# Performance work log

Hardware: AMD Instinct MI355X
Metric: run time of the kernel (lower is better)

## Reference

```python
import jax, jax.numpy as jnp
import numpy as np

D_MODEL = 768; D_KV = 64; H = 12; D_FF = 3072; L = 2
TP = 4; SP = 16; MT = 16; MS = 4
MASK_RATE = 0.2; EPS = 1e-6
B = 256; T = 64; F = 64
ST = (T // TP) * (F // SP)  # 64 tokens


def ln(x, s, b):
    mu = jnp.mean(x, -1, keepdims=True)
    var = jnp.mean(jnp.square(x - mu), -1, keepdims=True)
    return (x - mu) * jax.lax.rsqrt(var + EPS) * s + b


def mha(x, Wq, bq, Wk, bk, Wv, bv, Wo, bo):
    Bz, S, D = x.shape
    q = (x @ Wq + bq).reshape(Bz, S, H, D_KV)
    k = (x @ Wk + bk).reshape(Bz, S, H, D_KV)
    v = (x @ Wv + bv).reshape(Bz, S, H, D_KV)
    scores = jnp.einsum('bqhd,bkhd->bhqk', q, k) * (D_KV ** -0.5)
    attn = jax.nn.softmax(scores, axis=-1)
    o = jnp.einsum('bhqk,bkhd->bqhd', attn, v).reshape(Bz, S, H * D_KV)
    return o @ Wo + bo


def setup_inputs():
    key = jax.random.key(0)
    ks = jax.random.split(key, 16)
    s = 0.02
    nrm = lambda k, shp: jax.random.normal(k, shp, jnp.float32) * s
    return {
        'inputs': jax.random.normal(ks[0], (B, T, F, 1), jnp.float32),
        'randomness': jax.random.uniform(ks[1], (B * ST, 3), jnp.float32),
        'perm': jax.random.permutation(ks[2], B * ST),
        'conv_w': nrm(ks[3], (TP, SP, 1, D_MODEL)), 'conv_b': jnp.zeros((D_MODEL,)),
        'temp_embd': nrm(ks[4], (MT, D_MODEL)), 'spec_embd': nrm(ks[5], (MS, D_MODEL)),
        'pos_ln_s': jnp.ones((D_MODEL,)), 'pos_ln_b': jnp.zeros((D_MODEL,)),
        'mask_tok': nrm(ks[6], (D_MODEL,)), 'agg_tok': nrm(ks[7], (D_MODEL,)),
        'Wq': nrm(ks[8], (L, D_MODEL, H * D_KV)), 'bq': jnp.zeros((L, H * D_KV)),
        'Wk': nrm(ks[9], (L, D_MODEL, H * D_KV)), 'bk': jnp.zeros((L, H * D_KV)),
        'Wv': nrm(ks[10], (L, D_MODEL, H * D_KV)), 'bv': jnp.zeros((L, H * D_KV)),
        'Wo': nrm(ks[11], (L, H * D_KV, D_MODEL)), 'bo': jnp.zeros((L, D_MODEL)),
        'ln1_s': jnp.ones((L, D_MODEL)), 'ln1_b': jnp.zeros((L, D_MODEL)),
        'W1': nrm(ks[12], (L, D_MODEL, D_FF)), 'b1': jnp.zeros((L, D_FF)),
        'W2': nrm(ks[13], (L, D_FF, D_MODEL)), 'b2': jnp.zeros((L, D_MODEL)),
        'ln2_s': jnp.ones((L, D_MODEL)), 'ln2_b': jnp.zeros((L, D_MODEL)),
    }


def reference(inputs, randomness, perm, conv_w, conv_b, temp_embd, spec_embd,
              pos_ln_s, pos_ln_b, mask_tok, agg_tok, Wq, bq, Wk, bk, Wv, bv,
              Wo, bo, ln1_s, ln1_b, W1, b1, W2, b2, ln2_s, ln2_b):
    # Conv2D patchify: [B, T, F, 1] -> [B, T/4, F/16, d_model]
    x = jax.lax.conv_general_dilated(
        inputs, conv_w, (TP, SP), 'VALID',
        dimension_numbers=('NHWC', 'HWIO', 'NHWC')) + conv_b
    Bz, Tt, Ss, D = x.shape
    e = x.reshape(Bz, Tt * Ss, D)  # token embeddings [B, 64, 768]
    # Vectorized BERT-style random masking (replaces the per-element sparse-scatter loop)
    sel = randomness[:, 0] <= MASK_RATE
    m = (sel & (randomness[:, 1] <= 0.8)).astype(e.dtype).reshape(Bz, Tt * Ss)
    rnd = (sel & (randomness[:, 1] > 0.8) & (randomness[:, 2] <= 0.5)).astype(e.dtype).reshape(Bz, Tt * Ss)
    shuffled = jax.lax.stop_gradient(e.reshape(-1, D))[perm].reshape(Bz, Tt * Ss, D)
    me = e * (1.0 - m - rnd)[..., None] + mask_tok * m[..., None] + shuffled * rnd[..., None]
    # Spectro-temporal position embeddings + LN
    pos = (temp_embd[:Tt, None, :] + spec_embd[None, :Ss, :]).reshape(Tt * Ss, D)
    h = ln(me + pos, pos_ln_s, pos_ln_b)
    # Prepend AGG token
    h = jnp.concatenate([jnp.broadcast_to(agg_tok, (Bz, 1, D)), h], axis=1)
    # Post-norm transformer encoder
    for l in range(L):
        a = mha(h, Wq[l], bq[l], Wk[l], bk[l], Wv[l], bv[l], Wo[l], bo[l])
        h = ln(h + a, ln1_s[l], ln1_b[l])
        f = jax.nn.gelu(h @ W1[l] + b1[l], approximate=False) @ W2[l] + b2[l]
        h = ln(h + f, ln2_s[l], ln2_b[l])
    return h  # last_hidden_states [B, 65, 768]; aggregated=h[:,0], predictions=h[:,1:]
```

## Files before the change

kernel.cpp:

```cpp
#include <hip/hip_runtime.h>
#include <hip/hip_bf16.h>
#include <math.h>

using bf16 = __hip_bfloat16;
typedef __bf16 bf16x8v __attribute__((ext_vector_type(8)));
typedef float f32x4 __attribute__((ext_vector_type(4)));
typedef unsigned short ushort4v __attribute__((ext_vector_type(4)));

__device__ __forceinline__ float b2f(bf16 x) { return __bfloat162float(x); }
__device__ __forceinline__ bf16 f2b(float x) { return __float2bfloat16(x); }

__device__ __forceinline__ void gload_lds16(const void* g, void* l) {
  __builtin_amdgcn_global_load_lds(
      (__attribute__((address_space(1))) void*)(void*)g,
      (__attribute__((address_space(3))) void*)l, 16, 0, 0);
}

__device__ __forceinline__ float block_sum(float v, float* buf) {
  #pragma unroll
  for (int off = 32; off > 0; off >>= 1) v += __shfl_xor(v, off);
  __syncthreads();
  if ((threadIdx.x & 63) == 0) buf[threadIdx.x >> 6] = v;
  __syncthreads();
  return buf[0] + buf[1] + buf[2] + buf[3];
}

__global__ __launch_bounds__(256) void transpose_kernel(
    const float* __restrict__ in, bf16* __restrict__ out, int K, int N) {
  __shared__ float tile[32][33];
  const int nbx = N >> 5;
  const int bx = blockIdx.x % nbx, by = blockIdx.x / nbx;
  const int tx = threadIdx.x & 31, ty = threadIdx.x >> 5;
  #pragma unroll
  for (int i = 0; i < 4; ++i) {
    const int r = by * 32 + ty + i * 8;
    tile[ty + i * 8][tx] = in[(size_t)r * N + bx * 32 + tx];
  }
  __syncthreads();
  #pragma unroll
  for (int i = 0; i < 4; ++i) {
    const int r = bx * 32 + ty + i * 8;
    out[(size_t)r * K + by * 32 + tx] = f2b(tile[tx][ty + i * 8]);
  }
}

__global__ __launch_bounds__(256) void biasqkv_kernel(
    const float* __restrict__ bq, const float* __restrict__ bk,
    const float* __restrict__ bv, float* __restrict__ out) {
  const int i = blockIdx.x * 256 + threadIdx.x;
  if (i >= 2 * 2304) return;
  const int l = i / 2304, n = i % 2304;
  float v = (n < 768) ? bq[l * 768 + n]
          : (n < 1536) ? bk[l * 768 + n - 768] : bv[l * 768 + n - 1536];
  out[i] = v;
}

__global__ __launch_bounds__(256) void patchify_kernel(
    const float* __restrict__ in, const float* __restrict__ w,
    const float* __restrict__ cb, bf16* __restrict__ e) {
  __shared__ float patch[8][64];
  const int tid = threadIdx.x;
  const int tok0 = blockIdx.x * 8;
  for (int idx = tid; idx < 512; idx += 256) {
    const int t = idx >> 6, p = idx & 63;
    const int tok = tok0 + t;
    const int b = tok >> 6, t2 = tok & 63, tt = t2 >> 2, ss = t2 & 3;
    const int kt = p >> 4, kf = p & 15;
    patch[t][p] = in[((size_t)b * 64 + tt * 4 + kt) * 64 + ss * 16 + kf];
  }
  __syncthreads();
  for (int i = 0; i < 3; ++i) {
    const int d = tid + i * 256;
    const float cbv = cb[d];
    float acc[8];
    #pragma unroll
    for (int t = 0; t < 8; ++t) acc[t] = cbv;
    for (int p = 0; p < 64; ++p) {
      const float wv = w[p * 768 + d];
      #pragma unroll
      for (int t = 0; t < 8; ++t) acc[t] += patch[t][p] * wv;
    }
    #pragma unroll
    for (int t = 0; t < 8; ++t) e[(size_t)(tok0 + t) * 768 + d] = f2b(acc[t]);
  }
}

__global__ __launch_bounds__(256) void embed_kernel(
    const bf16* __restrict__ e, const float* __restrict__ randomness,
    const int* __restrict__ perm, const float* __restrict__ temp_embd,
    const float* __restrict__ spec_embd, const float* __restrict__ pls,
    const float* __restrict__ plb, const float* __restrict__ mask_tok,
    const float* __restrict__ agg_tok, bf16* __restrict__ h) {
  __shared__ float rbuf[4];
  const int row = blockIdx.x;
  const int b = row / 65, s = row % 65;
  const int tid = threadIdx.x;
  const size_t ob = (size_t)row * 768;
  if (s == 0) {
    #pragma unroll
    for (int i = 0; i < 3; ++i) { const int d = tid + i * 256; h[ob + d] = f2b(agg_tok[d]); }
    return;
  }
  const int tok = s - 1;
  const int gt = b * 64 + tok;
  const float r0 = randomness[gt * 3 + 0];
  const float r1 = randomness[gt * 3 + 1];
  const float r2 = randomness[gt * 3 + 2];
  const bool selb = (r0 <= 0.2f);
  const bool mflag = selb && (r1 <= 0.8f);
  const bool rflag = selb && (r1 > 0.8f) && (r2 <= 0.5f);
  const int src = rflag ? perm[gt] : gt;
  const int tt = tok >> 2, ss2 = tok & 3;
  float v[3]; float sum = 0.f;
  #pragma unroll
  for (int i = 0; i < 3; ++i) {
    const int d = tid + i * 256;
    const float ev = mflag ? mask_tok[d] : b2f(e[(size_t)src * 768 + d]);
    v[i] = ev + temp_embd[tt * 768 + d] + spec_embd[ss2 * 768 + d];
    sum += v[i];
  }
  const float mu = block_sum(sum, rbuf) * (1.f / 768.f);
  float q = 0.f;
  #pragma unroll
  for (int i = 0; i < 3; ++i) { const float t = v[i] - mu; q += t * t; }
  const float rstd = rsqrtf(block_sum(q, rbuf) * (1.f / 768.f) + 1e-6f);
  #pragma unroll
  for (int i = 0; i < 3; ++i) {
    const int d = tid + i * 256;
    h[ob + d] = f2b((v[i] - mu) * rstd * pls[d] + plb[d]);
  }
}

template <int F32OUT>
__global__ __launch_bounds__(256) void resln_kernel(
    const bf16* __restrict__ x, const bf16* __restrict__ y,
    const float* __restrict__ sc, const float* __restrict__ bi,
    void* __restrict__ outp) {
  __shared__ float rbuf[4];
  const int tid = threadIdx.x;
  const size_t base = (size_t)blockIdx.x * 768;
  float v[3]; float s = 0.f;
  #pragma unroll
  for (int i = 0; i < 3; ++i) {
    const int d = tid + i * 256;
    v[i] = b2f(x[base + d]) + b2f(y[base + d]);
    s += v[i];
  }
  const float mu = block_sum(s, rbuf) * (1.f / 768.f);
  float q = 0.f;
  #pragma unroll
  for (int i = 0; i < 3; ++i) { const float t = v[i] - mu; q += t * t; }
  const float rstd = rsqrtf(block_sum(q, rbuf) * (1.f / 768.f) + 1e-6f);
  #pragma unroll
  for (int i = 0; i < 3; ++i) {
    const int d = tid + i * 256;
    const float o = (v[i] - mu) * rstd * sc[d] + bi[d];
    if (F32OUT) ((float*)outp)[base + d] = o;
    else        ((bf16*)outp)[base + d] = f2b(o);
  }
}

template <int ACT>
__global__ __launch_bounds__(256, 2) void gemm_bt_kernel(
    const unsigned short* __restrict__ A, const unsigned short* __restrict__ BT,
    const float* __restrict__ bias, bf16* __restrict__ C, int N, int K) {
  __shared__ __align__(16) unsigned short lA[128 * 32];
  __shared__ __align__(16) unsigned short lB[128 * 32];
  const int tid = threadIdx.x;
  const int wid = tid >> 6, lane = tid & 63;
  const int nbn = N >> 7;
  const int bm = blockIdx.x / nbn, bn = blockIdx.x % nbn;
  const int wm = (wid >> 1) << 6, wn = (wid & 1) << 6;

  const size_t Kb = (size_t)K * 2;
  const char* gA = (const char*)A + (size_t)bm * 128 * Kb;
  const char* gB = (const char*)BT + (size_t)bn * 128 * Kb;
  const int r0 = tid >> 2;
  const int c0 = (tid & 3) * 16;
  char* lAw = (char*)lA + wid * 1024;
  char* lBw = (char*)lB + wid * 1024;

  const f32x4 z = {0.f, 0.f, 0.f, 0.f};
  f32x4 acc[4][4];
  #pragma unroll
  for (int i = 0; i < 4; ++i)
    #pragma unroll
    for (int j = 0; j < 4; ++j) acc[i][j] = z;

  const int frow = lane & 15;
  const int koff = (lane >> 4) * 8;

  for (int k0 = 0; k0 < K; k0 += 32) {
    const char* ga = gA + (size_t)k0 * 2 + c0;
    const char* gb = gB + (size_t)k0 * 2 + c0;
    gload_lds16(ga + (size_t)r0 * Kb, lAw);
    gload_lds16(ga + (size_t)(r0 + 64) * Kb, lAw + 4096);
    gload_lds16(gb + (size_t)r0 * Kb, lBw);
    gload_lds16(gb + (size_t)(r0 + 64) * Kb, lBw + 4096);
    __syncthreads();
    bf16x8v af[4], bfv[4];
    #pragma unroll
    for (int m = 0; m < 4; ++m)
      af[m] = *(const bf16x8v*)&lA[(wm + m * 16 + frow) * 32 + koff];
    #pragma unroll
    for (int n = 0; n < 4; ++n)
      bfv[n] = *(const bf16x8v*)&lB[(wn + n * 16 + frow) * 32 + koff];
    #pragma unroll
    for (int m = 0; m < 4; ++m)
      #pragma unroll
      for (int n = 0; n < 4; ++n)
        acc[m][n] = __builtin_amdgcn_mfma_f32_16x16x32_bf16(af[m], bfv[n], acc[m][n], 0, 0, 0);
    __syncthreads();
  }

  const int row0 = bm * 128 + wm + ((lane >> 4) << 2);
  const int col0 = bn * 128 + wn + frow;
  #pragma unroll
  for (int n = 0; n < 4; ++n) {
    const int col = col0 + n * 16;
    const float bv = bias[col];
    #pragma unroll
    for (int m = 0; m < 4; ++m) {
      const int row = row0 + m * 16;
      #pragma unroll
      for (int r = 0; r < 4; ++r) {
        float v = acc[m][n][r] + bv;
        if (ACT == 1) v = 0.5f * v * (1.0f + erff(v * 0.70710678f));
        C[(size_t)(row + r) * N + col] = f2b(v);
      }
    }
  }
}

__global__ __launch_bounds__(320) void attn_mfma_kernel(
    const bf16* __restrict__ qkv, bf16* __restrict__ ctx) {
  __shared__ __align__(16) bf16 sK[80][72];
  __shared__ __align__(16) bf16 sVt[64][104];
  __shared__ __align__(16) bf16 sP[5][16][104];
  const int b = blockIdx.x / 12, h = blockIdx.x % 12;
  const int tid = threadIdx.x;
  const int wave = tid >> 6, lane = tid & 63;
  const size_t base = ((size_t)b * 65) * 2304 + (size_t)h * 64;
  const bf16 bzero = f2b(0.f);

  for (int idx = tid; idx < 65 * 16; idx += 320) {
    const int row = idx >> 4, d4 = (idx & 15) * 4;
    const ushort4v kv = *(const ushort4v*)(qkv + base + (size_t)row * 2304 + 768 + d4);
    const ushort4v vv = *(const ushort4v*)(qkv + base + (size_t)row * 2304 + 1536 + d4);
    *(ushort4v*)&sK[row][d4] = kv;
    #pragma unroll
    for (int j = 0; j < 4; ++j) ((unsigned short*)&sVt[d4 + j][row])[0] = vv[j];
  }
  for (int idx = tid; idx < 15 * 16; idx += 320) {
    const int row = 65 + (idx >> 4), d4 = (idx & 15) * 4;
    *(ushort4v*)&sK[row][d4] = ushort4v{0, 0, 0, 0};
  }
  for (int idx = tid; idx < 64 * 8; idx += 320) {
    const int d = idx >> 3, c4 = 64 + (idx & 7) * 4;
    (void)d; (void)c4;
  }
  for (int idx = tid; idx < 64 * 31; idx += 320) {
    const int d = idx / 31, c = 65 + (idx % 31);
    sVt[d][c] = bzero;
  }
  __syncthreads();

  const int frow = lane & 15;
  const int koff = (lane >> 4) * 8;
  const int row0 = wave * 16;
  const int qrow = (row0 + frow > 64) ? 64 : (row0 + frow);
  const bf16* qptr = qkv + base + (size_t)qrow * 2304;
  const bf16x8v aq0 = *(const bf16x8v*)(qptr + koff);
  const bf16x8v aq1 = *(const bf16x8v*)(qptr + 32 + koff);

  const f32x4 z4 = {0.f, 0.f, 0.f, 0.f};
  f32x4 sacc[5];
  #pragma unroll
  for (int n = 0; n < 5; ++n) sacc[n] = z4;
  #pragma unroll
  for (int n = 0; n < 5; ++n) {
    const bf16x8v b0 = *(const bf16x8v*)&sK[n * 16 + frow][koff];
    const bf16x8v b1 = *(const bf16x8v*)&sK[n * 16 + frow][32 + koff];
    sacc[n] = __builtin_amdgcn_mfma_f32_16x16x32_bf16(aq0, b0, sacc[n], 0, 0, 0);
    sacc[n] = __builtin_amdgcn_mfma_f32_16x16x32_bf16(aq1, b1, sacc[n], 0, 0, 0);
  }

  #pragma unroll
  for (int r = 0; r < 4; ++r) {
    const int prow = ((lane >> 4) << 2) + r;
    float v[5];
    float mx = -1e30f;
    #pragma unroll
    for (int n = 0; n < 5; ++n) {
      const int col = n * 16 + frow;
      v[n] = (col < 65) ? sacc[n][r] * 0.125f : -1e30f;
      mx = fmaxf(mx, v[n]);
    }
    #pragma unroll
    for (int off = 1; off < 16; off <<= 1) mx = fmaxf(mx, __shfl_xor(mx, off));
    float sum = 0.f;
    #pragma unroll
    for (int n = 0; n < 5; ++n) { v[n] = __expf(v[n] - mx); sum += v[n]; }
    #pragma unroll
    for (int off = 1; off < 16; off <<= 1) sum += __shfl_xor(sum, off);
    const float inv = 1.f / sum;
    #pragma unroll
    for (int n = 0; n < 5; ++n)
      sP[wave][prow][n * 16 + frow] = f2b(v[n] * inv);
    sP[wave][prow][80 + frow] = bzero;
  }

  f32x4 oacc[4];
  #pragma unroll
  for (int n = 0; n < 4; ++n) oacc[n] = z4;
  #pragma unroll
  for (int kk = 0; kk < 3; ++kk) {
    const bf16x8v ap = *(const bf16x8v*)&sP[wave][frow][kk * 32 + koff];
    #pragma unroll
    for (int n = 0; n < 4; ++n) {
      const bf16x8v bv = *(const bf16x8v*)&sVt[n * 16 + frow][kk * 32 + koff];
      oacc[n] = __builtin_amdgcn_mfma_f32_16x16x32_bf16(ap, bv, oacc[n], 0, 0, 0);
    }
  }

  #pragma unroll
  for (int r = 0; r < 4; ++r) {
    const int row = row0 + ((lane >> 4) << 2) + r;
    if (row < 65) {
      bf16* op = ctx + ((size_t)b * 65 + row) * 768 + (size_t)h * 64 + frow;
      #pragma unroll
      for (int n = 0; n < 4; ++n) op[n * 16] = f2b(oacc[n][r]);
    }
  }
}

extern "C" void kernel_launch(void* const* d_in, const int* in_sizes, int n_in,
                              void* d_out, int out_size, void* d_ws, size_t ws_size,
                              hipStream_t stream) {
  (void)in_sizes; (void)n_in; (void)out_size; (void)ws_size;
  const float* inputs     = (const float*)d_in[0];
  const float* randomness = (const float*)d_in[1];
  const int*   perm       = (const int*)d_in[2];
  const float* conv_w     = (const float*)d_in[3];
  const float* conv_b     = (const float*)d_in[4];
  const float* temp_embd  = (const float*)d_in[5];
  const float* spec_embd  = (const float*)d_in[6];
  const float* pos_ln_s   = (const float*)d_in[7];
  const float* pos_ln_b   = (const float*)d_in[8];
  const float* mask_tok   = (const float*)d_in[9];
  const float* agg_tok    = (const float*)d_in[10];
  const float* Wq = (const float*)d_in[11]; const float* bq = (const float*)d_in[12];
  const float* Wk = (const float*)d_in[13]; const float* bk = (const float*)d_in[14];
  const float* Wv = (const float*)d_in[15]; const float* bv = (const float*)d_in[16];
  const float* Wo = (const float*)d_in[17]; const float* bo = (const float*)d_in[18];
  const float* ln1_s = (const float*)d_in[19]; const float* ln1_b = (const float*)d_in[20];
  const float* W1 = (const float*)d_in[21]; const float* b1 = (const float*)d_in[22];
  const float* W2 = (const float*)d_in[23]; const float* b2 = (const float*)d_in[24];
  const float* ln2_s = (const float*)d_in[25]; const float* ln2_b = (const float*)d_in[26];

  char* wsb = (char*)d_ws;
  size_t off = 0;
  auto carve = [&](size_t bytes) { char* p = wsb + off; off = (off + bytes + 255) & ~(size_t)255; return p; };
  bf16* wqkvT = (bf16*)carve((size_t)2 * 2304 * 768 * 2);
  bf16* woT   = (bf16*)carve((size_t)2 * 768 * 768 * 2);
  bf16* w1T   = (bf16*)carve((size_t)2 * 3072 * 768 * 2);
  bf16* w2T   = (bf16*)carve((size_t)2 * 768 * 3072 * 2);
  float* bqkv = (float*)carve((size_t)2 * 2304 * 4);
  bf16* ebuf  = (bf16*)carve((size_t)16640 * 768 * 2);
  bf16* hbuf  = (bf16*)carve((size_t)16640 * 768 * 2);
  bf16* qkvb  = (bf16*)carve((size_t)16640 * 2304 * 2);
  bf16* ctxb  = (bf16*)carve((size_t)16640 * 768 * 2);
  bf16* tmpb  = ebuf;
  bf16* midb  = qkvb;

  const dim3 blk(256);
  for (int l = 0; l < 2; ++l) {
    transpose_kernel<<<576, blk, 0, stream>>>(Wq + (size_t)l * 768 * 768, wqkvT + (size_t)l * 2304 * 768, 768, 768);
    transpose_kernel<<<576, blk, 0, stream>>>(Wk + (size_t)l * 768 * 768, wqkvT + (size_t)l * 2304 * 768 + 768 * 768, 768, 768);
    transpose_kernel<<<576, blk, 0, stream>>>(Wv + (size_t)l * 768 * 768, wqkvT + (size_t)l * 2304 * 768 + 2 * 768 * 768, 768, 768);
    transpose_kernel<<<576, blk, 0, stream>>>(Wo + (size_t)l * 768 * 768, woT + (size_t)l * 768 * 768, 768, 768);
    transpose_kernel<<<2304, blk, 0, stream>>>(W1 + (size_t)l * 768 * 3072, w1T + (size_t)l * 3072 * 768, 768, 3072);
    transpose_kernel<<<2304, blk, 0, stream>>>(W2 + (size_t)l * 3072 * 768, w2T + (size_t)l * 768 * 3072, 3072, 768);
  }
  biasqkv_kernel<<<18, blk, 0, stream>>>(bq, bk, bv, bqkv);
  patchify_kernel<<<2048, blk, 0, stream>>>(inputs, conv_w, conv_b, ebuf);
  embed_kernel<<<16640, blk, 0, stream>>>(ebuf, randomness, perm, temp_embd, spec_embd,
                                          pos_ln_s, pos_ln_b, mask_tok, agg_tok, hbuf);
  for (int l = 0; l < 2; ++l) {
    gemm_bt_kernel<0><<<130 * 18, blk, 0, stream>>>(
        (const unsigned short*)hbuf, (const unsigned short*)(wqkvT + (size_t)l * 2304 * 768),
        bqkv + l * 2304, qkvb, 2304, 768);
    attn_mfma_kernel<<<256 * 12, dim3(320), 0, stream>>>(qkvb, ctxb);
    gemm_bt_kernel<0><<<130 * 6, blk, 0, stream>>>(
        (const unsigned short*)ctxb, (const unsigned short*)(woT + (size_t)l * 768 * 768),
        bo + l * 768, tmpb, 768, 768);
    resln_kernel<0><<<16640, blk, 0, stream>>>(hbuf, tmpb, ln1_s + l * 768, ln1_b + l * 768, hbuf);
    gemm_bt_kernel<1><<<130 * 24, blk, 0, stream>>>(
        (const unsigned short*)hbuf, (const unsigned short*)(w1T + (size_t)l * 3072 * 768),
        b1 + l * 3072, midb, 3072, 768);
    gemm_bt_kernel<0><<<130 * 6, blk, 0, stream>>>(
        (const unsigned short*)midb, (const unsigned short*)(w2T + (size_t)l * 768 * 3072),
        b2 + l * 768, tmpb, 768, 3072);
    if (l == 1)
      resln_kernel<1><<<16640, blk, 0, stream>>>(hbuf, tmpb, ln2_s + l * 768, ln2_b + l * 768, d_out);
    else
      resln_kernel<0><<<16640, blk, 0, stream>>>(hbuf, tmpb, ln2_s + l * 768, ln2_b + l * 768, hbuf);
  }
}
```

Baseline: 1.052 ms.

## Replace GEMM with 256-row double-buffered tiles, swizzled LDS, XCD remap, staged stores

Replaces the 128x128 single-buffered GEMM with a 512-thread kernel using 256-row tiles (256 or 128 columns), a K-step of 64, and double-buffered global-to-LDS loads so loads overlap MFMA compute. LDS reads use an XOR swizzle to avoid bank conflicts. Workgroup IDs are remapped across the 8 XCDs so neighbouring tiles share L2. The epilogue stages results through LDS to issue coalesced 16-byte stores. The larger tiles cut redundant A/B traffic, but raise register and LDS use, which may limit occupancy.

```diff
diff --git a/kernel.cpp b/kernel.cpp
--- a/kernel.cpp
+++ b/kernel.cpp
@@ -6,6 +6,7 @@
 typedef __bf16 bf16x8v __attribute__((ext_vector_type(8)));
 typedef float f32x4 __attribute__((ext_vector_type(4)));
 typedef unsigned short ushort4v __attribute__((ext_vector_type(4)));
+typedef unsigned short ushort8v __attribute__((ext_vector_type(8)));
 
 __device__ __forceinline__ float b2f(bf16 x) { return __bfloat162float(x); }
 __device__ __forceinline__ bf16 f2b(float x) { return __float2bfloat16(x); }
@@ -160,75 +161,132 @@
   }
 }
 
-template <int ACT>
-__global__ __launch_bounds__(256, 2) void gemm_bt_kernel(
+template <int WN, int ACT>
+__global__ __launch_bounds__(512, 2) void gemm256_kernel(
     const unsigned short* __restrict__ A, const unsigned short* __restrict__ BT,
-    const float* __restrict__ bias, bf16* __restrict__ C, int N, int K) {
-  __shared__ __align__(16) unsigned short lA[128 * 32];
-  __shared__ __align__(16) unsigned short lB[128 * 32];
+    const float* __restrict__ bias, bf16* __restrict__ C, int N, int K, int nbn) {
+  constexpr int WM = 8 / WN;
+  constexpr int RPW = 256 / WM;
+  constexpr int BN = 64 * WN;
+  constexpr int MF = RPW / 16;
+  constexpr int NF = 4;
+  constexpr int ABYTES = 256 * 128;
+  constexpr int BBYTES = BN * 128;
+  constexpr int PADC = BN + 4;
+  constexpr int LOOPB = 2 * (ABYTES + BBYTES);
+  constexpr int EPIB = 256 * PADC * 2;
+  constexpr int SMEMB = LOOPB > EPIB ? LOOPB : EPIB;
+  __shared__ __align__(16) char smem[SMEMB];
+
+  const int nwg = gridDim.x;
+  const int orig = blockIdx.x;
+  const int q8 = nwg >> 3, r8 = nwg & 7;
+  const int xcd = orig & 7, lin = orig >> 3;
+  const int bid = (xcd < r8 ? xcd * (q8 + 1) : r8 * (q8 + 1) + (xcd - r8) * q8) + lin;
+  const int bm = bid / nbn, bn = bid % nbn;
+
   const int tid = threadIdx.x;
-  const int wid = tid >> 6, lane = tid & 63;
-  const int nbn = N >> 7;
-  const int bm = blockIdx.x / nbn, bn = blockIdx.x % nbn;
-  const int wm = (wid >> 1) << 6, wn = (wid & 1) << 6;
+  const int w = tid >> 6, lane = tid & 63;
+  const int wrow = w / WN, wcol = w % WN;
+  const int frow = lane & 15;
+  const int kgrp = lane & 48;
 
   const size_t Kb = (size_t)K * 2;
-  const char* gA = (const char*)A + (size_t)bm * 128 * Kb;
-  const char* gB = (const char*)BT + (size_t)bn * 128 * Kb;
-  const int r0 = tid >> 2;
-  const int c0 = (tid & 3) * 16;
-  char* lAw = (char*)lA + wid * 1024;
-  char* lBw = (char*)lB + wid * 1024;
-
-  const f32x4 z = {0.f, 0.f, 0.f, 0.f};
-  f32x4 acc[4][4];
-  #pragma unroll
-  for (int i = 0; i < 4; ++i)
-    #pragma unroll
-    for (int j = 0; j < 4; ++j) acc[i][j] = z;
-
-  const int frow = lane & 15;
-  const int koff = (lane >> 4) * 8;
-
-  for (int k0 = 0; k0 < K; k0 += 32) {
-    const char* ga = gA + (size_t)k0 * 2 + c0;
-    const char* gb = gB + (size_t)k0 * 2 + c0;
-    gload_lds16(ga + (size_t)r0 * Kb, lAw);
-    gload_lds16(ga + (size_t)(r0 + 64) * Kb, lAw + 4096);
-    gload_lds16(gb + (size_t)r0 * Kb, lBw);
-    gload_lds16(gb + (size_t)(r0 + 64) * Kb, lBw + 4096);
+  const int laneRow = lane >> 3;
+  const int laneCB = ((lane & 7) << 4) ^ (lane & 32);
+  const char* gA = (const char*)A + ((size_t)bm * 256 + w * 8 + laneRow) * Kb + laneCB;
+  const char* gB = (const char*)BT + ((size_t)bn * BN + w * 8 + laneRow) * Kb + laneCB;
+
+  f32x4 acc[MF][NF];
+  #pragma unroll
+  for (int i = 0; i < MF; ++i)
+    #pragma unroll
+    for (int j = 0; j < NF; ++j) acc[i][j] = f32x4{0.f, 0.f, 0.f, 0.f};
+
+  auto stage = [&](int buf, int kt) {
+    const size_t ko = (size_t)kt << 7;
+    char* la = smem + buf * (ABYTES + BBYTES);
+    char* lb = la + ABYTES;
+    #pragma unroll
+    for (int i = 0; i < 4; ++i)
+      gload_lds16(gA + (size_t)i * 64 * Kb + ko, la + i * 8192 + w * 1024);
+    #pragma unroll
+    for (int i = 0; i < BN / 64; ++i)
+      gload_lds16(gB + (size_t)i * 64 * Kb + ko, lb + i * 8192 + w * 1024);
+  };
+
+  auto compute = [&](int buf) {
+    const char* la = smem + buf * (ABYTES + BBYTES);
+    const char* lb = la + ABYTES;
+    #pragma unroll
+    for (int mq = 0; mq < MF / 4; ++mq) {
+      bf16x8v af[4][2];
+      #pragma unroll
+      for (int j = 0; j < 4; ++j)
+        #pragma unroll
+        for (int s = 0; s < 2; ++s) {
+          const int row = wrow * RPW + (mq * 4 + j) * 16 + frow;
+          const int cb = (s * 64 + kgrp) ^ (((row >> 2) & 1) << 5);
+          af[j][s] = *(const bf16x8v*)(la + row * 128 + cb);
+        }
+      #pragma unroll
+      for (int nq = 0; nq < 2; ++nq) {
+        bf16x8v bv[2][2];
+        #pragma unroll
+        for (int n = 0; n < 2; ++n)
+          #pragma unroll
+          for (int s = 0; s < 2; ++s) {
+            const int row = wcol * 64 + (nq * 2 + n) * 16 + frow;
+            const int cb = (s * 64 + kgrp) ^ (((row >> 2) & 1) << 5);
+            bv[n][s] = *(const bf16x8v*)(lb + row * 128 + cb);
+          }
+        #pragma unroll
+        for (int j = 0; j < 4; ++j)
+          #pragma unroll
+          for (int n = 0; n < 2; ++n) {
+            acc[mq * 4 + j][nq * 2 + n] = __builtin_amdgcn_mfma_f32_16x16x32_bf16(
+                af[j][0], bv[n][0], acc[mq * 4 + j][nq * 2 + n], 0, 0, 0);
+            acc[mq * 4 + j][nq * 2 + n] = __builtin_amdgcn_mfma_f32_16x16x32_bf16(
+                af[j][1], bv[n][1], acc[mq * 4 + j][nq * 2 + n], 0, 0, 0);
+          }
+      }
+    }
+  };
+
+  const int NT = K >> 6;
+  stage(0, 0);
+  __syncthreads();
+  int cur = 0;
+  for (int t = 0; t < NT; ++t) {
+    if (t + 1 < NT) stage(cur ^ 1, t + 1);
+    compute(cur);
     __syncthreads();
-    bf16x8v af[4], bfv[4];
-    #pragma unroll
-    for (int m = 0; m < 4; ++m)
-      af[m] = *(const bf16x8v*)&lA[(wm + m * 16 + frow) * 32 + koff];
-    #pragma unroll
-    for (int n = 0; n < 4; ++n)
-      bfv[n] = *(const bf16x8v*)&lB[(wn + n * 16 + frow) * 32 + koff];
-    #pragma unroll
-    for (int m = 0; m < 4; ++m)
-      #pragma unroll
-      for (int n = 0; n < 4; ++n)
-        acc[m][n] = __builtin_amdgcn_mfma_f32_16x16x32_bf16(af[m], bfv[n], acc[m][n], 0, 0, 0);
-    __syncthreads();
-  }
-
-  const int row0 = bm * 128 + wm + ((lane >> 4) << 2);
-  const int col0 = bn * 128 + wn + frow;
-  #pragma unroll
-  for (int n = 0; n < 4; ++n) {
-    const int col = col0 + n * 16;
-    const float bv = bias[col];
-    #pragma unroll
-    for (int m = 0; m < 4; ++m) {
-      const int row = row0 + m * 16;
+    cur ^= 1;
+  }
+
+  bf16* cb16 = (bf16*)smem;
+  #pragma unroll
+  for (int mf = 0; mf < MF; ++mf)
+    #pragma unroll
+    for (int nf = 0; nf < NF; ++nf) {
+      const int col = wcol * 64 + nf * 16 + frow;
+      const float bvv = bias[bn * BN + col];
       #pragma unroll
       for (int r = 0; r < 4; ++r) {
-        float v = acc[m][n][r] + bv;
+        const int row = wrow * RPW + mf * 16 + ((lane >> 4) << 2) + r;
+        float v = acc[mf][nf][r] + bvv;
         if (ACT == 1) v = 0.5f * v * (1.0f + erff(v * 0.70710678f));
-        C[(size_t)(row + r) * N + col] = f2b(v);
+        cb16[row * PADC + col] = f2b(v);
       }
     }
+  __syncthreads();
+  constexpr int CPR = BN / 8;
+  #pragma unroll
+  for (int j = 0; j < 256 * CPR / 512; ++j) {
+    const int idx = tid + j * 512;
+    const int row = idx / CPR, c = idx % CPR;
+    const ushort8v val = *(const ushort8v*)(cb16 + row * PADC + c * 8);
+    *(ushort8v*)(C + ((size_t)bm * 256 + row) * N + bn * BN + c * 8) = val;
   }
 }
 
@@ -254,10 +312,6 @@
   for (int idx = tid; idx < 15 * 16; idx += 320) {
     const int row = 65 + (idx >> 4), d4 = (idx & 15) * 4;
     *(ushort4v*)&sK[row][d4] = ushort4v{0, 0, 0, 0};
-  }
-  for (int idx = tid; idx < 64 * 8; idx += 320) {
-    const int d = idx >> 3, c4 = 64 + (idx & 7) * 4;
-    (void)d; (void)c4;
   }
   for (int idx = tid; idx < 64 * 31; idx += 320) {
     const int d = idx / 31, c = 65 + (idx % 31);
@@ -387,20 +441,20 @@
   embed_kernel<<<16640, blk, 0, stream>>>(ebuf, randomness, perm, temp_embd, spec_embd,
                                           pos_ln_s, pos_ln_b, mask_tok, agg_tok, hbuf);
   for (int l = 0; l < 2; ++l) {
-    gemm_bt_kernel<0><<<130 * 18, blk, 0, stream>>>(
+    gemm256_kernel<4, 0><<<65 * 9, dim3(512), 0, stream>>>(
         (const unsigned short*)hbuf, (const unsigned short*)(wqkvT + (size_t)l * 2304 * 768),
-        bqkv + l * 2304, qkvb, 2304, 768);
+        bqkv + l * 2304, qkvb, 2304, 768, 9);
     attn_mfma_kernel<<<256 * 12, dim3(320), 0, stream>>>(qkvb, ctxb);
-    gemm_bt_kernel<0><<<130 * 6, blk, 0, stream>>>(
+    gemm256_kernel<2, 0><<<65 * 6, dim3(512), 0, stream>>>(
         (const unsigned short*)ctxb, (const unsigned short*)(woT + (size_t)l * 768 * 768),
-        bo + l * 768, tmpb, 768, 768);
+        bo + l * 768, tmpb, 768, 768, 6);
     resln_kernel<0><<<16640, blk, 0, stream>>>(hbuf, tmpb, ln1_s + l * 768, ln1_b + l * 768, hbuf);
-    gemm_bt_kernel<1><<<130 * 24, blk, 0, stream>>>(
+    gemm256_kernel<4, 1><<<65 * 12, dim3(512), 0, stream>>>(
         (const unsigned short*)hbuf, (const unsigned short*)(w1T + (size_t)l * 3072 * 768),
-        b1 + l * 3072, midb, 3072, 768);
-    gemm_bt_kernel<0><<<130 * 6, blk, 0, stream>>>(
+        b1 + l * 3072, midb, 3072, 768, 12);
+    gemm256_kernel<2, 0><<<65 * 6, dim3(512), 0, stream>>>(
         (const unsigned short*)midb, (const unsigned short*)(w2T + (size_t)l * 768 * 3072),
-        b2 + l * 768, tmpb, 768, 3072);
+        b2 + l * 768, tmpb, 768, 3072, 6);
     if (l == 1)
       resln_kernel<1><<<16640, blk, 0, stream>>>(hbuf, tmpb, ln2_s + l * 768, ln2_b + l * 768, d_out);
     else
```

Result: faster. 966.9 us (-8.1%).
